# Performance work log

Measured on AMD Instinct MI355X. Metric: run time of the kernel, lower is better.

Reference implementation:

```python
import jax, jax.numpy as jnp
import numpy as np

NUM_HEADS = 16
NEG_INF = jnp.float32(-1e9)


def setup_inputs() -> dict:
    key = jax.random.key(0)
    ks = jax.random.split(key, 4)
    B, N, C = 2, 2048, 1024
    s_in = 1.0 / np.sqrt(C)
    return {
        "x": jax.random.normal(ks[0], (B, N, C), jnp.float32),
        "attention_mask": jnp.ones((B, N, N), jnp.int32),
        "qkv_w": jax.random.normal(ks[1], (3 * C, C), jnp.float32) * s_in,
        "qkv_b": jnp.zeros((3 * C,), jnp.float32),
        "proj_w": jax.random.normal(ks[2], (C, C), jnp.float32) * s_in,
        "proj_b": jnp.zeros((C,), jnp.float32),
    }


def reference(x, attention_mask, qkv_w, qkv_b, proj_w, proj_b):
    B, N, C = x.shape
    H = NUM_HEADS
    D = C // H
    scale = D ** -0.5
    # fused QKV projection (torch Linear: x @ W^T + b)
    qkv = (x @ qkv_w.T + qkv_b).reshape(B, N, 3, H, D)
    qkv = jnp.transpose(qkv, (2, 0, 3, 1, 4))  # [3, B, H, N, D]
    q, k, v = qkv[0], qkv[1], qkv[2]
    # scaled dot-product scores [B, H, N, N]
    attn = jnp.einsum("bhnd,bhmd->bhnm", q, k) * scale
    # padding mask: [B, N, N] broadcast over heads
    attn = jnp.where(attention_mask[:, None, :, :] == 0, NEG_INF, attn)
    # causal mask
    causal = jnp.triu(jnp.ones((N, N), bool), k=1)
    attn = jnp.where(causal, NEG_INF, attn)
    w = jax.nn.softmax(attn, axis=-1)
    out = jnp.einsum("bhnm,bhmd->bhnd", w, v)
    out = jnp.transpose(out, (0, 2, 1, 3)).reshape(B, N, C)
    return out @ proj_w.T + proj_b
```

## Files before the change

kernel.cpp:

```cpp
#include <hip/hip_runtime.h>
#include <hip/hip_bf16.h>


typedef __bf16 bf16x8 __attribute__((ext_vector_type(8)));
typedef __bf16 bf16x4 __attribute__((ext_vector_type(4)));
typedef __bf16 bf16x2 __attribute__((ext_vector_type(2)));
typedef float  f32x4  __attribute__((ext_vector_type(4)));
typedef float  f32x16 __attribute__((ext_vector_type(16)));
typedef int    i32x4  __attribute__((ext_vector_type(4)));

#define MFMA16(a, b, c) __builtin_amdgcn_mfma_f32_16x16x32_bf16((a), (b), (c), 0, 0, 0)

__device__ __forceinline__ void async_copy16(const __bf16* g, __bf16* l) {
    __builtin_amdgcn_global_load_lds(
        (const __attribute__((address_space(1))) void*)g,
        (__attribute__((address_space(3))) void*)l,
        16, 0, 0);
}

__device__ __forceinline__ unsigned packbf(float a, float b) {
    union { bf16x2 v; unsigned u; } un;
    un.v[0] = (__bf16)a; un.v[1] = (__bf16)b;
    return un.u;
}

__global__ void f32_to_bf16_k(const float* __restrict__ in, __bf16* __restrict__ out, int n4) {
    int i = blockIdx.x * blockDim.x + threadIdx.x;
    if (i >= n4) return;
    float4 v = reinterpret_cast<const float4*>(in)[i];
    bf16x4 o;
    o[0] = (__bf16)v.x; o[1] = (__bf16)v.y; o[2] = (__bf16)v.z; o[3] = (__bf16)v.w;
    reinterpret_cast<bf16x4*>(out)[i] = o;
}

__global__ void mask_reduce_k(const int* __restrict__ mask, int* __restrict__ mflag) {
    __shared__ int ok;
    const int t = threadIdx.x;
    if (t == 0) ok = 1;
    __syncthreads();
    const int jt = blockIdx.x & 31;
    const int it = (blockIdx.x >> 5) & 31;
    const int b  = blockIdx.x >> 10;
    bool all1 = true;
#pragma unroll
    for (int c = 0; c < 4; ++c) {
        const int row = c * 16 + (t >> 4);
        const int col = (t & 15) * 4;
        const int4 v = *reinterpret_cast<const int4*>(
            &mask[((size_t)(b * 2048 + it * 64 + row)) * 2048 + jt * 64 + col]);
        all1 = all1 && v.x && v.y && v.z && v.w;
    }
    if (!all1) ok = 0;
    __syncthreads();
    if (t == 0) mflag[(b * 32 + it) * 32 + jt] = ok;
}

#define BAR() asm volatile("s_barrier" ::: "memory")
#define VM2() asm volatile("s_waitcnt vmcnt(2)" ::: "memory")

__global__ __launch_bounds__(512, 2) void gemm_qkv8_k(
    const __bf16* __restrict__ A, const __bf16* __restrict__ Bm,
    const float* __restrict__ bias,
    __bf16* __restrict__ qg, __bf16* __restrict__ kg, __bf16* __restrict__ vtg)
{
    __shared__ __align__(16) __bf16 As[2][16384];
    __shared__ __align__(16) __bf16 Bs[2][16384];

    const int t = threadIdx.x;
    const int lane = t & 63;
    const int w = t >> 6;
    const int wr = w >> 2, wc = w & 3;
    const int li = lane & 15, g = lane >> 4;

    const int bid = (blockIdx.x & 7) * 24 + (blockIdx.x >> 3);
    const int m0 = (bid / 12) << 8;
    const int n0 = (bid % 12) << 8;

    const int srow = t >> 3;
    const int scol = ((t & 7) ^ (srow & 7)) << 3;
    const __bf16* pA = A  + (size_t)(m0 + srow) * 1024 + scol;
    const __bf16* pB = Bm + (size_t)(n0 + srow) * 1024 + scol;
    __bf16* dA = &As[0][0] + t * 8;
    __bf16* dB = &Bs[0][0] + t * 8;

#define STAGE_A(BB, T, HH) do {                                                   \
    const size_t ro_ = (size_t)((HH) * 128) * 1024 + (size_t)(T) * 64;            \
    async_copy16(pA + ro_,         dA + (BB) * 16384 + (HH) * 8192);              \
    async_copy16(pA + ro_ + 65536, dA + (BB) * 16384 + (HH) * 8192 + 4096);       \
  } while (0)
#define STAGE_B(BB, T, HH) do {                                                   \
    const size_t ro_ = (size_t)((HH) * 128) * 1024 + (size_t)(T) * 64;            \
    async_copy16(pB + ro_,         dB + (BB) * 16384 + (HH) * 8192);              \
    async_copy16(pB + ro_ + 65536, dB + (BB) * 16384 + (HH) * 8192 + 4096);       \
  } while (0)

    const int aoff0 = ((0 + g) ^ (li & 7)) << 3;
    const int aoff1 = ((4 + g) ^ (li & 7)) << 3;
    const int abase = (wr * 128 + li) * 64;
    const int bbase = (wc * 64 + li) * 64;

    f32x4 acc[8][4] = {};
    bf16x8 a[4][2], b[2][2][2];

#define READ_A(BB, MH) do { _Pragma("unroll")                                     \
    for (int mi2 = 0; mi2 < 4; ++mi2) {                                           \
      const __bf16* p_ = &As[BB][abase + ((MH) * 4 + mi2) * 1024];                \
      a[mi2][0] = *reinterpret_cast<const bf16x8*>(p_ + aoff0);                   \
      a[mi2][1] = *reinterpret_cast<const bf16x8*>(p_ + aoff1); } } while (0)
#define READ_B(BB, NH) do { _Pragma("unroll")                                     \
    for (int ni2 = 0; ni2 < 2; ++ni2) {                                           \
      const __bf16* p_ = &Bs[BB][bbase + ((NH) * 2 + ni2) * 1024];                \
      b[NH][ni2][0] = *reinterpret_cast<const bf16x8*>(p_ + aoff0);               \
      b[NH][ni2][1] = *reinterpret_cast<const bf16x8*>(p_ + aoff1); } } while (0)
#define MFMA_QUAD(MH, NH) do {                                                    \
    __builtin_amdgcn_s_setprio(1);                                                \
    _Pragma("unroll") for (int mi2 = 0; mi2 < 4; ++mi2)                           \
    _Pragma("unroll") for (int ni2 = 0; ni2 < 2; ++ni2) {                         \
      f32x4 c_ = acc[(MH) * 4 + mi2][(NH) * 2 + ni2];                             \
      c_ = MFMA16(a[mi2][0], b[NH][ni2][0], c_);                                  \
      c_ = MFMA16(a[mi2][1], b[NH][ni2][1], c_);                                  \
      acc[(MH) * 4 + mi2][(NH) * 2 + ni2] = c_; }                                 \
    __builtin_amdgcn_s_setprio(0); } while (0)

#define KTILE(BB, T) do {                                                         \
    const int Tn_  = ((T) + 1 < 16) ? (T) + 1 : 15;                               \
    const int Tn2_ = ((T) + 2 < 16) ? (T) + 2 : 15;                               \
    STAGE_A((BB) ^ 1, Tn_, 1);                                                    \
    READ_A(BB, 0); READ_B(BB, 0);                                                 \
    BAR(); MFMA_QUAD(0, 0); BAR();                                                \
    STAGE_B((BB) ^ 1, Tn_, 0);                                                    \
    READ_B(BB, 1);                                                                \
    BAR(); MFMA_QUAD(0, 1); BAR();                                                \
    STAGE_B((BB) ^ 1, Tn_, 1);                                                    \
    READ_A(BB, 1);                                                                \
    BAR(); MFMA_QUAD(1, 0); BAR();                                                \
    STAGE_A((BB), Tn2_, 0);                                                       \
    VM2(); BAR(); MFMA_QUAD(1, 1); BAR();                                         \
  } while (0)

    STAGE_A(0, 0, 0); STAGE_A(0, 0, 1);
    STAGE_B(0, 0, 0); STAGE_B(0, 0, 1);
    STAGE_A(1, 1, 0);
    VM2(); BAR();

#pragma unroll 1
    for (int jj = 0; jj < 8; ++jj) {
        KTILE(0, 2 * jj);
        KTILE(1, 2 * jj + 1);
    }

    const int nbase = n0 + wc * 64;
    const int s = nbase >> 10;
    const int headg = (m0 >> 11) * 16 + ((nbase & 1023) >> 6);
    const int mrow = (m0 & 2047) + wr * 128 + g * 4;
    float bv[4];
#pragma unroll
    for (int ni = 0; ni < 4; ++ni) bv[ni] = bias[nbase + ni * 16 + li];

    if (s == 2) {
#pragma unroll
        for (int mi = 0; mi < 8; ++mi) {
#pragma unroll
            for (int ni = 0; ni < 4; ++ni) {
                bf16x4 st;
#pragma unroll
                for (int r = 0; r < 4; ++r) st[r] = (__bf16)(acc[mi][ni][r] + bv[ni]);
                *reinterpret_cast<bf16x4*>(
                    &vtg[((size_t)(headg * 64) + ni * 16 + li) * 2048 + mrow + mi * 16]) = st;
            }
        }
    } else {
        __bf16* og = (s == 0) ? qg : kg;
        const float sc = (s == 0) ? 0.18033688f : 1.0f;
#pragma unroll
        for (int mi = 0; mi < 8; ++mi) {
#pragma unroll
            for (int r = 0; r < 4; ++r) {
                __bf16* rp = og + ((size_t)headg * 2048 + mrow + mi * 16 + r) * 64;
#pragma unroll
                for (int ni = 0; ni < 4; ++ni)
                    rp[ni * 16 + li] = (__bf16)((acc[mi][ni][r] + bv[ni]) * sc);
            }
        }
    }
#undef KTILE
#undef MFMA_QUAD
#undef READ_A
#undef READ_B
#undef STAGE_A
#undef STAGE_B
}

__global__ __launch_bounds__(256) void gemm_proj_k(
    const __bf16* __restrict__ A, const __bf16* __restrict__ Bm,
    const float* __restrict__ bias, int M, int N, int K,
    float* __restrict__ outf)
{
    __shared__ __align__(16) __bf16 As[128 * 64];
    __shared__ __align__(16) __bf16 Bs[128 * 64];
    const int t = threadIdx.x;
    const int nb = N >> 7;
    const int m0 = (blockIdx.x / nb) << 7;
    const int n0 = (blockIdx.x % nb) << 7;
    const int lane = t & 63, w = t >> 6;
    const int g = lane >> 4, li = lane & 15;
    const int wr = w >> 1, wc = w & 1;
    const __bf16* Ab = A + (size_t)m0 * K;
    const __bf16* Bb = Bm + (size_t)n0 * K;

    f32x4 acc[4][4] = {};

    for (int k0 = 0; k0 < K; k0 += 64) {
#pragma unroll
        for (int c = 0; c < 4; ++c) {
            const int e = (c * 256 + t) * 8;
            const int row = e >> 6;
            const int col = e & 63;
            async_copy16(Ab + (size_t)row * K + k0 + col, As + e);
            async_copy16(Bb + (size_t)row * K + k0 + col, Bs + e);
        }
        __syncthreads();
#pragma unroll
        for (int kk = 0; kk < 2; ++kk) {
            bf16x8 af[4], bf[4];
#pragma unroll
            for (int mi = 0; mi < 4; ++mi)
                af[mi] = *reinterpret_cast<const bf16x8*>(
                    &As[(wr * 64 + mi * 16 + li) * 64 + kk * 32 + g * 8]);
#pragma unroll
            for (int ni = 0; ni < 4; ++ni)
                bf[ni] = *reinterpret_cast<const bf16x8*>(
                    &Bs[(wc * 64 + ni * 16 + li) * 64 + kk * 32 + g * 8]);
#pragma unroll
            for (int mi = 0; mi < 4; ++mi)
#pragma unroll
                for (int ni = 0; ni < 4; ++ni)
                    acc[mi][ni] = MFMA16(af[mi], bf[ni], acc[mi][ni]);
        }
        __syncthreads();
    }

#pragma unroll
    for (int mi = 0; mi < 4; ++mi) {
#pragma unroll
        for (int ni = 0; ni < 4; ++ni) {
            const int n = n0 + wc * 64 + ni * 16 + li;
            const float bv = bias[n];
#pragma unroll
            for (int r = 0; r < 4; ++r) {
                const int m = m0 + wr * 64 + mi * 16 + g * 4 + r;
                outf[(size_t)m * N + n] = acc[mi][ni][r] + bv;
            }
        }
    }
}

__global__ __launch_bounds__(256) void attn_k(
    const __bf16* __restrict__ qg, const __bf16* __restrict__ kg,
    const __bf16* __restrict__ vtg, const int* __restrict__ mflag,
    const int* __restrict__ mask, __bf16* __restrict__ ao)
{
    __shared__ __align__(16) __bf16 Ks[2][4096];
    __shared__ __align__(16) __bf16 Vs[2][4096];
    __shared__ __align__(16) __bf16 Ps[4][1024];
    const int t = threadIdx.x;
    const int w = t >> 6, lane = t & 63;
    const int li = lane & 15, g = lane >> 4;
    const int xcd = blockIdx.x & 7;
    const int idx = blockIdx.x >> 3;
    const int hg  = xcd * 4 + (idx & 3);
    const int band = 31 - (idx >> 2);
    const int bI = hg >> 4, hI = hg & 15;
    const int iq = band * 64 + w * 16 + li;
    const int diag = band;
    const size_t hoff = (size_t)hg * (2048 * 64);
    const __bf16* qh = qg + hoff;
    const __bf16* kh = kg + hoff;
    const __bf16* vh = vtg + hoff;
    char* pw = (char*)&Ps[w][0];
    const int sw7 = li & 7;

    bf16x8 qf[2];
#pragma unroll
    for (int half = 0; half < 2; ++half)
        qf[half] = *reinterpret_cast<const bf16x8*>(&qh[(size_t)iq * 64 + half * 32 + g * 8]);

    f32x4 o[4] = {};
    float mrun = -1e30f, lrun = 0.0f;

#define STAGE(BUF, KT) do {                                                       \
    _Pragma("unroll")                                                             \
    for (int c_ = 0; c_ < 2; ++c_) {                                              \
        const int p_ = c_ * 4096 + t * 16;                                        \
        const int row_ = p_ >> 7, sl_ = (p_ >> 4) & 7;                            \
        const int gc_ = (sl_ ^ (row_ & 7)) << 3;                                  \
        async_copy16(kh + (size_t)(((KT) << 6) + row_) * 64 + gc_,                \
                     (__bf16*)((char*)(&Ks[BUF][0]) + p_));                       \
        async_copy16(vh + (size_t)row_ * 2048 + ((KT) << 6) + gc_,                \
                     (__bf16*)((char*)(&Vs[BUF][0]) + p_));                       \
    }                                                                             \
} while (0)

    int cur = 0;
    STAGE(0, 0);
    for (int kt = 0; kt <= diag; ++kt) {
        __syncthreads();
        if (kt < diag) STAGE(cur ^ 1, kt + 1);
        const char* kb = (char*)&Ks[cur][0];
        const char* vb = (char*)&Vs[cur][0];
        f32x4 s[4] = {};
        __builtin_amdgcn_s_setprio(1);
#pragma unroll
        for (int kb_ = 0; kb_ < 4; ++kb_) {
            const int row = kb_ * 16 + li;
#pragma unroll
            for (int half = 0; half < 2; ++half) {
                bf16x8 kf = *reinterpret_cast<const bf16x8*>(
                    kb + row * 128 + (((half * 4 + g) ^ sw7) << 4));
                s[kb_] = MFMA16(kf, qf[half], s[kb_]);
            }
        }
        __builtin_amdgcn_s_setprio(0);
        const bool pflag = (mflag[(bI * 32 + band) * 32 + kt] == 0);
        if (pflag || kt == diag) {
            const int jb = kt * 64;
#pragma unroll
            for (int kb_ = 0; kb_ < 4; ++kb_)
#pragma unroll
                for (int r = 0; r < 4; ++r) {
                    const int j0 = jb + kb_ * 16 + 4 * g + r;
                    float v0 = s[kb_][r];
                    if (j0 > iq || (pflag && mask[((size_t)(bI * 2048 + iq)) * 2048 + j0] == 0))
                        v0 = -1e30f;
                    s[kb_][r] = v0;
                }
        }
        float mt = fmaxf(fmaxf(s[0][0], s[0][1]), fmaxf(s[0][2], s[0][3]));
#pragma unroll
        for (int kb_ = 1; kb_ < 4; ++kb_) {
            mt = fmaxf(mt, fmaxf(fmaxf(s[kb_][0], s[kb_][1]), fmaxf(s[kb_][2], s[kb_][3])));
        }
        mt = fmaxf(mt, __shfl_xor(mt, 16));
        mt = fmaxf(mt, __shfl_xor(mt, 32));
        if (!__all(mt <= mrun + 8.0f)) {
            const float mn = fmaxf(mrun, mt);
            const float alpha = exp2f(mrun - mn);
#pragma unroll
            for (int df = 0; df < 4; ++df)
#pragma unroll
                for (int r = 0; r < 4; ++r) o[df][r] *= alpha;
            lrun *= alpha;
            mrun = mn;
        }
        float rs = 0.0f;
#pragma unroll
        for (int kb_ = 0; kb_ < 4; ++kb_)
#pragma unroll
            for (int r = 0; r < 4; ++r) {
                const float p = exp2f(s[kb_][r] - mrun);
                s[kb_][r] = p;
                rs += p;
            }
        rs += __shfl_xor(rs, 16);
        rs += __shfl_xor(rs, 32);
        lrun += rs;
#pragma unroll
        for (int kb_ = 0; kb_ < 4; ++kb_) {
            const unsigned lo = packbf(s[kb_][0], s[kb_][1]);
            const unsigned hi = packbf(s[kb_][2], s[kb_][3]);
            *reinterpret_cast<uint2*>(
                pw + li * 128 + (((2 * kb_ + (g >> 1)) ^ sw7) << 4) + ((g & 1) << 3)) =
                make_uint2(lo, hi);
        }
        bf16x8 pb[2];
#pragma unroll
        for (int ks = 0; ks < 2; ++ks)
            pb[ks] = *reinterpret_cast<const bf16x8*>(
                pw + li * 128 + (((4 * ks + g) ^ sw7) << 4));
        __builtin_amdgcn_s_setprio(1);
#pragma unroll
        for (int df = 0; df < 4; ++df) {
            const int vrow = df * 16 + li;
#pragma unroll
            for (int ks = 0; ks < 2; ++ks) {
                bf16x8 vf = *reinterpret_cast<const bf16x8*>(
                    vb + vrow * 128 + (((4 * ks + g) ^ sw7) << 4));
                o[df] = MFMA16(vf, pb[ks], o[df]);
            }
        }
        __builtin_amdgcn_s_setprio(0);
        cur ^= 1;
    }
#undef STAGE

    const float inv = 1.0f / lrun;
    __bf16* aor = ao + ((size_t)(bI * 2048 + iq)) * 1024 + hI * 64 + g * 4;
#pragma unroll
    for (int df = 0; df < 4; ++df) {
        bf16x4 st;
#pragma unroll
        for (int r = 0; r < 4; ++r) st[r] = (__bf16)(o[df][r] * inv);
        *reinterpret_cast<bf16x4*>(&aor[df * 16]) = st;
    }
}

extern "C" void kernel_launch(void* const* d_in, const int* in_sizes, int n_in,
                              void* d_out, int out_size, void* d_ws, size_t ws_size,
                              hipStream_t stream)
{
    const float* x      = (const float*)d_in[0];
    const int*   mask   = (const int*)d_in[1];
    const float* qkv_w  = (const float*)d_in[2];
    const float* qkv_b  = (const float*)d_in[3];
    const float* proj_w = (const float*)d_in[4];
    const float* proj_b = (const float*)d_in[5];
    float* out = (float*)d_out;

    char* ws = (char*)d_ws;
    __bf16* xb    = (__bf16*)(ws + 0);
    __bf16* wqkv  = (__bf16*)(ws + 8388608);
    __bf16* wproj = (__bf16*)(ws + 14680064);
    __bf16* qg    = (__bf16*)(ws + 16777216);
    __bf16* kg    = (__bf16*)(ws + 25165824);
    __bf16* vtg   = (__bf16*)(ws + 33554432);
    __bf16* ao    = (__bf16*)(ws + 41943040);
    int*    mflag = (int*)(ws + 50331648);

    f32_to_bf16_k<<<1048576 / 256, 256, 0, stream>>>(x, xb, 1048576);
    f32_to_bf16_k<<<786432 / 256, 256, 0, stream>>>(qkv_w, wqkv, 786432);
    f32_to_bf16_k<<<262144 / 256, 256, 0, stream>>>(proj_w, wproj, 262144);
    mask_reduce_k<<<2 * 32 * 32, 256, 0, stream>>>(mask, mflag);
    gemm_qkv8_k<<<192, 512, 0, stream>>>(xb, wqkv, qkv_b, qg, kg, vtg);
    attn_k<<<1024, 256, 0, stream>>>(qg, kg, vtg, mflag, mask, ao);
    gemm_proj_k<<<32 * 8, 256, 0, stream>>>(ao, wproj, proj_b, 4096, 1024, 1024, out);
}
```

Before: 138.2 us.

## Use 128-row query bands with 8 waves per attention block and merge conversion kernels

After: 137.9 us. About the same (-0.2%).

```diff
diff --git a/kernel.cpp b/kernel.cpp
--- a/kernel.cpp
+++ b/kernel.cpp
@@ -24,13 +24,20 @@
     return un.u;
 }
 
-__global__ void f32_to_bf16_k(const float* __restrict__ in, __bf16* __restrict__ out, int n4) {
+__global__ void f32_to_bf16_3k(const float* __restrict__ a, __bf16* __restrict__ ad, int na,
+                               const float* __restrict__ b, __bf16* __restrict__ bd, int nb,
+                               const float* __restrict__ c, __bf16* __restrict__ cd, int nc)
+{
     int i = blockIdx.x * blockDim.x + threadIdx.x;
-    if (i >= n4) return;
-    float4 v = reinterpret_cast<const float4*>(in)[i];
+    const float* src; __bf16* dst; int j;
+    if (i < na)            { src = a; dst = ad; j = i; }
+    else if (i < na + nb)  { src = b; dst = bd; j = i - na; }
+    else if (i < na + nb + nc) { src = c; dst = cd; j = i - na - nb; }
+    else return;
+    float4 v = reinterpret_cast<const float4*>(src)[j];
     bf16x4 o;
     o[0] = (__bf16)v.x; o[1] = (__bf16)v.y; o[2] = (__bf16)v.z; o[3] = (__bf16)v.w;
-    reinterpret_cast<bf16x4*>(out)[i] = o;
+    reinterpret_cast<bf16x4*>(dst)[j] = o;
 }
 
 __global__ void mask_reduce_k(const int* __restrict__ mask, int* __restrict__ mflag) {
@@ -255,24 +262,26 @@
     }
 }
 
-__global__ __launch_bounds__(256) void attn_k(
+__global__ __launch_bounds__(512) void attn_k(
     const __bf16* __restrict__ qg, const __bf16* __restrict__ kg,
     const __bf16* __restrict__ vtg, const int* __restrict__ mflag,
     const int* __restrict__ mask, __bf16* __restrict__ ao)
 {
     __shared__ __align__(16) __bf16 Ks[2][4096];
     __shared__ __align__(16) __bf16 Vs[2][4096];
-    __shared__ __align__(16) __bf16 Ps[4][1024];
+    __shared__ __align__(16) __bf16 Ps[8][1024];
     const int t = threadIdx.x;
     const int w = t >> 6, lane = t & 63;
     const int li = lane & 15, g = lane >> 4;
     const int xcd = blockIdx.x & 7;
     const int idx = blockIdx.x >> 3;
     const int hg  = xcd * 4 + (idx & 3);
-    const int band = 31 - (idx >> 2);
+    const int band = 15 - (idx >> 2);
     const int bI = hg >> 4, hI = hg & 15;
-    const int iq = band * 64 + w * 16 + li;
-    const int diag = band;
+    const int iq = band * 128 + w * 16 + li;
+    const int mydiag = 2 * band + (w >> 2);
+    const int ktmax = 2 * band + 1;
+    const int rowt = 2 * band + (w >> 2);
     const size_t hoff = (size_t)hg * (2048 * 64);
     const __bf16* qh = qg + hoff;
     const __bf16* kh = kg + hoff;
@@ -289,110 +298,108 @@
     float mrun = -1e30f, lrun = 0.0f;
 
 #define STAGE(BUF, KT) do {                                                       \
-    _Pragma("unroll")                                                             \
-    for (int c_ = 0; c_ < 2; ++c_) {                                              \
-        const int p_ = c_ * 4096 + t * 16;                                        \
-        const int row_ = p_ >> 7, sl_ = (p_ >> 4) & 7;                            \
-        const int gc_ = (sl_ ^ (row_ & 7)) << 3;                                  \
-        async_copy16(kh + (size_t)(((KT) << 6) + row_) * 64 + gc_,                \
-                     (__bf16*)((char*)(&Ks[BUF][0]) + p_));                       \
-        async_copy16(vh + (size_t)row_ * 2048 + ((KT) << 6) + gc_,                \
-                     (__bf16*)((char*)(&Vs[BUF][0]) + p_));                       \
-    }                                                                             \
+    const int p_ = t * 16;                                                        \
+    const int row_ = p_ >> 7, sl_ = (p_ >> 4) & 7;                                \
+    const int gc_ = (sl_ ^ (row_ & 7)) << 3;                                      \
+    async_copy16(kh + (size_t)(((KT) << 6) + row_) * 64 + gc_,                    \
+                 (__bf16*)((char*)(&Ks[BUF][0]) + p_));                           \
+    async_copy16(vh + (size_t)row_ * 2048 + ((KT) << 6) + gc_,                    \
+                 (__bf16*)((char*)(&Vs[BUF][0]) + p_));                           \
 } while (0)
 
     int cur = 0;
     STAGE(0, 0);
-    for (int kt = 0; kt <= diag; ++kt) {
+    for (int kt = 0; kt <= ktmax; ++kt) {
         __syncthreads();
-        if (kt < diag) STAGE(cur ^ 1, kt + 1);
-        const char* kb = (char*)&Ks[cur][0];
-        const char* vb = (char*)&Vs[cur][0];
-        f32x4 s[4] = {};
-        __builtin_amdgcn_s_setprio(1);
-#pragma unroll
-        for (int kb_ = 0; kb_ < 4; ++kb_) {
-            const int row = kb_ * 16 + li;
-#pragma unroll
-            for (int half = 0; half < 2; ++half) {
-                bf16x8 kf = *reinterpret_cast<const bf16x8*>(
-                    kb + row * 128 + (((half * 4 + g) ^ sw7) << 4));
-                s[kb_] = MFMA16(kf, qf[half], s[kb_]);
-            }
-        }
-        __builtin_amdgcn_s_setprio(0);
-        const bool pflag = (mflag[(bI * 32 + band) * 32 + kt] == 0);
-        if (pflag || kt == diag) {
-            const int jb = kt * 64;
+        if (kt < ktmax) STAGE(cur ^ 1, kt + 1);
+        if (kt <= mydiag) {
+            const char* kb = (char*)&Ks[cur][0];
+            const char* vb = (char*)&Vs[cur][0];
+            f32x4 s[4] = {};
+            __builtin_amdgcn_s_setprio(1);
+#pragma unroll
+            for (int kb_ = 0; kb_ < 4; ++kb_) {
+                const int row = kb_ * 16 + li;
+#pragma unroll
+                for (int half = 0; half < 2; ++half) {
+                    bf16x8 kf = *reinterpret_cast<const bf16x8*>(
+                        kb + row * 128 + (((half * 4 + g) ^ sw7) << 4));
+                    s[kb_] = MFMA16(kf, qf[half], s[kb_]);
+                }
+            }
+            __builtin_amdgcn_s_setprio(0);
+            const bool pflag = (mflag[(bI * 32 + rowt) * 32 + kt] == 0);
+            if (pflag || kt == mydiag) {
+                const int jb = kt * 64;
+#pragma unroll
+                for (int kb_ = 0; kb_ < 4; ++kb_)
+#pragma unroll
+                    for (int r = 0; r < 4; ++r) {
+                        const int j0 = jb + kb_ * 16 + 4 * g + r;
+                        float v0 = s[kb_][r];
+                        if (j0 > iq ||
+                            (pflag && mask[((size_t)(bI * 2048 + iq)) * 2048 + j0] == 0))
+                            v0 = -1e30f;
+                        s[kb_][r] = v0;
+                    }
+            }
+            float mt = fmaxf(fmaxf(s[0][0], s[0][1]), fmaxf(s[0][2], s[0][3]));
+#pragma unroll
+            for (int kb_ = 1; kb_ < 4; ++kb_)
+                mt = fmaxf(mt, fmaxf(fmaxf(s[kb_][0], s[kb_][1]),
+                                     fmaxf(s[kb_][2], s[kb_][3])));
+            mt = fmaxf(mt, __shfl_xor(mt, 16));
+            mt = fmaxf(mt, __shfl_xor(mt, 32));
+            if (!__all(mt <= mrun + 8.0f)) {
+                const float mn = fmaxf(mrun, mt);
+                const float alpha = exp2f(mrun - mn);
+#pragma unroll
+                for (int df = 0; df < 4; ++df)
+#pragma unroll
+                    for (int r = 0; r < 4; ++r) o[df][r] *= alpha;
+                lrun *= alpha;
+                mrun = mn;
+            }
 #pragma unroll
             for (int kb_ = 0; kb_ < 4; ++kb_)
 #pragma unroll
                 for (int r = 0; r < 4; ++r) {
-                    const int j0 = jb + kb_ * 16 + 4 * g + r;
-                    float v0 = s[kb_][r];
-                    if (j0 > iq || (pflag && mask[((size_t)(bI * 2048 + iq)) * 2048 + j0] == 0))
-                        v0 = -1e30f;
-                    s[kb_][r] = v0;
+                    const float p = exp2f(s[kb_][r] - mrun);
+                    s[kb_][r] = p;
+                    lrun += p;
                 }
-        }
-        float mt = fmaxf(fmaxf(s[0][0], s[0][1]), fmaxf(s[0][2], s[0][3]));
-#pragma unroll
-        for (int kb_ = 1; kb_ < 4; ++kb_) {
-            mt = fmaxf(mt, fmaxf(fmaxf(s[kb_][0], s[kb_][1]), fmaxf(s[kb_][2], s[kb_][3])));
-        }
-        mt = fmaxf(mt, __shfl_xor(mt, 16));
-        mt = fmaxf(mt, __shfl_xor(mt, 32));
-        if (!__all(mt <= mrun + 8.0f)) {
-            const float mn = fmaxf(mrun, mt);
-            const float alpha = exp2f(mrun - mn);
-#pragma unroll
-            for (int df = 0; df < 4; ++df)
-#pragma unroll
-                for (int r = 0; r < 4; ++r) o[df][r] *= alpha;
-            lrun *= alpha;
-            mrun = mn;
-        }
-        float rs = 0.0f;
-#pragma unroll
-        for (int kb_ = 0; kb_ < 4; ++kb_)
-#pragma unroll
-            for (int r = 0; r < 4; ++r) {
-                const float p = exp2f(s[kb_][r] - mrun);
-                s[kb_][r] = p;
-                rs += p;
-            }
-        rs += __shfl_xor(rs, 16);
-        rs += __shfl_xor(rs, 32);
-        lrun += rs;
-#pragma unroll
-        for (int kb_ = 0; kb_ < 4; ++kb_) {
-            const unsigned lo = packbf(s[kb_][0], s[kb_][1]);
-            const unsigned hi = packbf(s[kb_][2], s[kb_][3]);
-            *reinterpret_cast<uint2*>(
-                pw + li * 128 + (((2 * kb_ + (g >> 1)) ^ sw7) << 4) + ((g & 1) << 3)) =
-                make_uint2(lo, hi);
-        }
-        bf16x8 pb[2];
-#pragma unroll
-        for (int ks = 0; ks < 2; ++ks)
-            pb[ks] = *reinterpret_cast<const bf16x8*>(
-                pw + li * 128 + (((4 * ks + g) ^ sw7) << 4));
-        __builtin_amdgcn_s_setprio(1);
-#pragma unroll
-        for (int df = 0; df < 4; ++df) {
-            const int vrow = df * 16 + li;
-#pragma unroll
-            for (int ks = 0; ks < 2; ++ks) {
-                bf16x8 vf = *reinterpret_cast<const bf16x8*>(
-                    vb + vrow * 128 + (((4 * ks + g) ^ sw7) << 4));
-                o[df] = MFMA16(vf, pb[ks], o[df]);
-            }
-        }
-        __builtin_amdgcn_s_setprio(0);
+#pragma unroll
+            for (int kb_ = 0; kb_ < 4; ++kb_) {
+                const unsigned lo = packbf(s[kb_][0], s[kb_][1]);
+                const unsigned hi = packbf(s[kb_][2], s[kb_][3]);
+                *reinterpret_cast<uint2*>(
+                    pw + li * 128 + (((2 * kb_ + (g >> 1)) ^ sw7) << 4) + ((g & 1) << 3)) =
+                    make_uint2(lo, hi);
+            }
+            bf16x8 pb[2];
+#pragma unroll
+            for (int ks = 0; ks < 2; ++ks)
+                pb[ks] = *reinterpret_cast<const bf16x8*>(
+                    pw + li * 128 + (((4 * ks + g) ^ sw7) << 4));
+            __builtin_amdgcn_s_setprio(1);
+#pragma unroll
+            for (int df = 0; df < 4; ++df) {
+                const int vrow = df * 16 + li;
+#pragma unroll
+                for (int ks = 0; ks < 2; ++ks) {
+                    bf16x8 vf = *reinterpret_cast<const bf16x8*>(
+                        vb + vrow * 128 + (((4 * ks + g) ^ sw7) << 4));
+                    o[df] = MFMA16(vf, pb[ks], o[df]);
+                }
+            }
+            __builtin_amdgcn_s_setprio(0);
+        }
         cur ^= 1;
     }
 #undef STAGE
 
+    lrun += __shfl_xor(lrun, 16);
+    lrun += __shfl_xor(lrun, 32);
     const float inv = 1.0f / lrun;
     __bf16* aor = ao + ((size_t)(bI * 2048 + iq)) * 1024 + hI * 64 + g * 4;
 #pragma unroll
@@ -426,11 +433,11 @@
     __bf16* ao    = (__bf16*)(ws + 41943040);
     int*    mflag = (int*)(ws + 50331648);
 
-    f32_to_bf16_k<<<1048576 / 256, 256, 0, stream>>>(x, xb, 1048576);
-    f32_to_bf16_k<<<786432 / 256, 256, 0, stream>>>(qkv_w, wqkv, 786432);
-    f32_to_bf16_k<<<262144 / 256, 256, 0, stream>>>(proj_w, wproj, 262144);
+    f32_to_bf16_3k<<<8192, 256, 0, stream>>>(x, xb, 1048576,
+                                             qkv_w, wqkv, 786432,
+                                             proj_w, wproj, 262144);
     mask_reduce_k<<<2 * 32 * 32, 256, 0, stream>>>(mask, mflag);
     gemm_qkv8_k<<<192, 512, 0, stream>>>(xb, wqkv, qkv_b, qg, kg, vtg);
-    attn_k<<<1024, 256, 0, stream>>>(qg, kg, vtg, mflag, mask, ao);
+    attn_k<<<512, 512, 0, stream>>>(qg, kg, vtg, mflag, mask, ao);
     gemm_proj_k<<<32 * 8, 256, 0, stream>>>(ao, wproj, proj_b, 4096, 1024, 1024, out);
 }
```
